# Kernel optimization log

Measured on AMD Instinct MI355X. Metric: run time of the kernel, lower is better.

Reference implementation:

```python
import jax, jax.numpy as jnp
import numpy as np

UNITS = 512
MEM = 16384
IN_DIM = 512
BATCH = 64
USAGE_DECAY = 0.95


def _hard_sigmoid(x):
    # keras hard_sigmoid: clip(0.2*x + 0.5, 0, 1)
    return jnp.clip(0.2 * x + 0.5, 0.0, 1.0)


def _l2norm(x, axis):
    # K.l2_normalize with eps guard
    return x * jax.lax.rsqrt(jnp.maximum(jnp.sum(x * x, axis=axis, keepdims=True), 1e-12))


def setup_inputs() -> dict:
    key = jax.random.key(0)
    ks = jax.random.split(key, 10)
    bias = jnp.concatenate([
        jnp.zeros((UNITS,), jnp.float32),
        jnp.ones((UNITS,), jnp.float32),   # unit_forget_bias
        jnp.zeros((2 * UNITS,), jnp.float32),
    ])
    return {
        "inputs": jax.random.normal(ks[0], (BATCH, IN_DIM), jnp.float32),
        "h_tm1": jax.random.normal(ks[1], (BATCH, UNITS), jnp.float32) * 0.1,
        "c_tm1": jax.random.normal(ks[2], (BATCH, UNITS), jnp.float32) * 0.1,
        "r_tm1": jax.random.normal(ks[3], (BATCH, UNITS), jnp.float32) * 0.1,
        "m_tm1": jax.random.normal(ks[4], (MEM, UNITS), jnp.float32),
        "c_wu_tm1": jax.random.uniform(ks[5], (MEM, BATCH), jnp.float32),
        "c_wlu_tm1": jax.random.uniform(ks[6], (MEM, BATCH), jnp.float32),
        "c_wr_tm1": jax.random.uniform(ks[7], (MEM, BATCH), jnp.float32),
        "kernel": jax.random.normal(ks[8], (IN_DIM, 4 * UNITS), jnp.float32) * 0.02,
        "recurrent_kernel": jax.random.normal(ks[9], (UNITS, 5 * UNITS), jnp.float32) * 0.02,
        "bias": bias,
        "write_gate": jnp.zeros((1,), jnp.float32),
    }


def reference(inputs, h_tm1, c_tm1, r_tm1, m_tm1, c_wu_tm1, c_wlu_tm1, c_wr_tm1,
              kernel, recurrent_kernel, bias, write_gate):
    u = UNITS
    # --- LSTM gates (no dropout / inference path) ---
    x = inputs @ kernel + bias                         # (B, 4U)
    x_i, x_f, x_c, x_o = jnp.split(x, 4, axis=-1)
    hk = h_tm1 @ recurrent_kernel[:, :4 * u]           # (B, 4U)
    h_i, h_f, h_c, h_o = jnp.split(hk, 4, axis=-1)
    r_i = r_tm1 @ recurrent_kernel[:, 4 * u:]          # read vector feeds input gate
    i_g = _hard_sigmoid(x_i + h_i + r_i)
    f_g = _hard_sigmoid(x_f + h_f)
    c = f_g * c_tm1 + i_g * jnp.tanh(x_c + h_c)
    o_g = _hard_sigmoid(x_o + h_o)
    h = o_g * jnp.tanh(c)                              # (B, U)

    # --- external memory addressing ---
    key_list = h.T                                     # (U, B)
    wg = jax.nn.sigmoid(write_gate)                    # (1,)
    # faithful to source: additive c_wlu_tm1 term (no multiply)
    c_ww = wg * c_wr_tm1 + (1.0 - wg) + c_wlu_tm1      # (M, B)
    n_key = _l2norm(key_list, 0)                       # (U, B)
    n_mem = _l2norm(m_tm1, 1)                          # (M, U)
    cos = n_mem @ n_key                                # (M, B)
    # faithful: K.softmax default axis=-1 => softmax over batch axis
    c_wr = jax.nn.softmax(cos, axis=-1)                # (M, B)
    read = (m_tm1.T @ c_wr).T                          # (B, U)
    c_wu = USAGE_DECAY * c_wu_tm1 + c_wr + c_ww        # (M, B)

    # least-used slot per batch column (top_k with k=M, take last => min)
    nth_smallest = jnp.min(c_wu, axis=0)               # (B,)
    nth_smallest_i = jnp.argmin(c_wu, axis=0)          # (B,)
    c_wlu = (c_wu <= nth_smallest[None, :]).astype(jnp.float32)  # (M, B)

    # zero the least-used rows, then write keys weighted by c_ww
    keep = jnp.prod(1.0 - jax.nn.one_hot(nth_smallest_i, MEM, dtype=jnp.float32), axis=0)  # (M,)
    m = m_tm1 * keep[:, None] + c_ww @ h               # (M, U)

    return h, c, read, m, c_wu, c_wlu, c_wr
```

## Files before the change

kernel.cpp:

```cpp
#include <hip/hip_runtime.h>
#include <math.h>

#define OUT_H    0
#define OUT_C    32768
#define OUT_READ 65536
#define OUT_M    98304
#define OUT_CWU  8486912
#define OUT_CWLU 9535488
#define OUT_CWR  10584064

#define WS_NKF   0
#define WS_HBF   16384
#define WS_PMIN  32768
#define WS_PIDX  49152
#define WS_MINF  65536
#define WS_IDXF  65600
#define WS_CWWF  65664
#define WS_CWRF  589952
#define WS_RPART 1114240

typedef short bf16x8 __attribute__((ext_vector_type(8)));
typedef float f32x4  __attribute__((ext_vector_type(4)));

__device__ __forceinline__ float hsig(float x) {
    return fminf(fmaxf(0.2f * x + 0.5f, 0.f), 1.f);
}
__device__ __forceinline__ unsigned short f2bf(float x) {
    unsigned u = __float_as_uint(x);
    return (unsigned short)((u + 0x7fffu + ((u >> 16) & 1u)) >> 16);
}

__global__ __launch_bounds__(256) void k_preact(
    const float* __restrict__ inputs, const float* __restrict__ h_tm1,
    const float* __restrict__ r_tm1, const float* __restrict__ wk,
    const float* __restrict__ rk, float* __restrict__ pre)
{
    __shared__ alignas(16) unsigned short Afr[8192];
    __shared__ alignas(16) unsigned short Bfr[8192];
    const int cb = blockIdx.x % 72, kh = blockIdx.x / 72;
    const int vcol0 = cb * 64;
    const float* A; const float* W; int wstride, wcol0;
    if (vcol0 < 2048)      { A = inputs; W = wk; wstride = 2048; wcol0 = vcol0; }
    else if (vcol0 < 4096) { A = h_tm1;  W = rk; wstride = 2560; wcol0 = vcol0 - 2048; }
    else                   { A = r_tm1;  W = rk; wstride = 2560; wcol0 = 2048 + (vcol0 - 4096); }
    const int tid = threadIdx.x;
    const int w = tid >> 6, lane = tid & 63;
    const int lhi = lane >> 4, llo = lane & 15;

    {
        const int koct = tid & 15;
        const int s = koct >> 2;
        #pragma unroll
        for (int i = 0; i < 4; ++i) {
            int row = i * 16 + (tid >> 4);
            const float* src = &A[row * 512 + kh * 128 + koct * 8];
            float4 x0 = *(const float4*)src;
            float4 x1 = *(const float4*)&src[4];
            int ln = (row & 15) + 16 * (koct & 3);
            int rt = row >> 4;
            union { unsigned short hx[8]; uint4 v; } pk;
            pk.hx[0] = f2bf(x0.x); pk.hx[1] = f2bf(x0.y);
            pk.hx[2] = f2bf(x0.z); pk.hx[3] = f2bf(x0.w);
            pk.hx[4] = f2bf(x1.x); pk.hx[5] = f2bf(x1.y);
            pk.hx[6] = f2bf(x1.z); pk.hx[7] = f2bf(x1.w);
            *(uint4*)&Afr[((s * 4 + rt) * 64 + ln) << 3] = pk.v;
        }
    }
    #pragma unroll
    for (int q = 0; q < 8; ++q) {
        int idx = q * 256 + tid;
        int krow = idx >> 4;
        int c4 = (idx & 15) * 4;
        float4 wv = *(const float4*)&W[(size_t)(kh * 128 + krow) * wstride + wcol0 + c4];
        int s = krow >> 5, lh = (krow & 31) >> 3, e = krow & 7;
        float ws4[4] = { wv.x, wv.y, wv.z, wv.w };
        #pragma unroll
        for (int j = 0; j < 4; ++j) {
            int col = c4 + j;
            int tc = col >> 4;
            int ln = (col & 15) + 16 * lh;
            Bfr[(((s * 4 + tc) * 64 + ln) << 3) + e] = f2bf(ws4[j]);
        }
    }
    __syncthreads();

    f32x4 acc[4] = {};
    #pragma unroll
    for (int s = 0; s < 4; ++s) {
        bf16x8 af = *(const bf16x8*)&Afr[((s * 4 + w) * 64 + lane) << 3];
        #pragma unroll
        for (int tc = 0; tc < 4; ++tc) {
            bf16x8 bf = *(const bf16x8*)&Bfr[((s * 4 + tc) * 64 + lane) << 3];
            acc[tc] = __builtin_amdgcn_mfma_f32_16x16x32_bf16(af, bf, acc[tc], 0, 0, 0);
        }
    }

    float* dst = pre + (size_t)kh * 294912;
    #pragma unroll
    for (int tc = 0; tc < 4; ++tc) {
        #pragma unroll
        for (int reg = 0; reg < 4; ++reg) {
            int row = w * 16 + lhi * 4 + reg;
            dst[row * 4608 + vcol0 + tc * 16 + llo] = acc[tc][reg];
        }
    }
}

__global__ __launch_bounds__(256) void k_gates(
    const float* __restrict__ pre, const float* __restrict__ bias,
    const float* __restrict__ c_tm1, float* __restrict__ out,
    unsigned short* __restrict__ nkf, unsigned short* __restrict__ hbf)
{
    int b = blockIdx.x, t = threadIdx.x;
    const float* p0 = pre + b * 4608;
    const float* p1 = pre + 294912 + b * 4608;
    const float* p2 = pre + 2 * 294912 + b * 4608;
    const float* p3 = pre + 3 * 294912 + b * 4608;
    float hh[2], cc[2];
    #pragma unroll
    for (int q = 0; q < 2; ++q) {
        int u = t + q * 256;
        #define S4(o) (p0[o] + p1[o] + p2[o] + p3[o])
        float xi = S4(u)        + bias[u];
        float xf = S4(512 + u)  + bias[512 + u];
        float xc = S4(1024 + u) + bias[1024 + u];
        float xo = S4(1536 + u) + bias[1536 + u];
        float hi = S4(2048 + u);
        float hf = S4(2560 + u);
        float hc = S4(3072 + u);
        float ho = S4(3584 + u);
        float ri = S4(4096 + u);
        #undef S4
        float ig = hsig(xi + hi + ri);
        float fg = hsig(xf + hf);
        cc[q] = fg * c_tm1[b * 512 + u] + ig * tanhf(xc + hc);
        float og = hsig(xo + ho);
        hh[q] = og * tanhf(cc[q]);
        out[OUT_H + b * 512 + u] = hh[q];
        out[OUT_C + b * 512 + u] = cc[q];
    }
    float ss = hh[0] * hh[0] + hh[1] * hh[1];
    __shared__ float red[4];
    for (int m = 1; m < 64; m <<= 1) ss += __shfl_xor(ss, m);
    if ((t & 63) == 0) red[t >> 6] = ss;
    __syncthreads();
    float tot = red[0] + red[1] + red[2] + red[3];
    float rn = rsqrtf(fmaxf(tot, 1e-12f));
    #pragma unroll
    for (int q = 0; q < 2; ++q) {
        int u = t + q * 256;
        int s = u >> 5, n = b >> 4;
        int lane = (b & 15) + 16 * ((u & 31) >> 3);
        int e = u & 7;
        nkf[(((s * 4 + n) * 64 + lane) << 3) + e] = f2bf(hh[q] * rn);
        int s2 = b >> 5, N = u >> 4;
        int l2 = (u & 15) + 16 * ((b & 31) >> 3);
        int e2 = b & 7;
        hbf[(((s2 * 32 + N) * 64 + l2) << 3) + e2] = f2bf(hh[q]);
    }
}

__global__ __launch_bounds__(256) void k_cos(
    const float* __restrict__ m_tm1, const unsigned short* __restrict__ nkf,
    const float* __restrict__ cwr_tm1, const float* __restrict__ cwlu_tm1,
    const float* __restrict__ cwu_tm1, const float* __restrict__ wgp,
    float* out, float* __restrict__ pmin, int* __restrict__ pidx,
    unsigned short* __restrict__ cwwf, unsigned short* __restrict__ cwrf)
{
    __shared__ alignas(16) unsigned short Af[2048 * 8];
    __shared__ float rn[64];
    __shared__ float pmv[4][64];
    __shared__ int   pmi[4][64];
    const int row0 = blockIdx.x * 64;
    const int tid = threadIdx.x;
    const int w = tid >> 6, lane = tid & 63;
    f32x4 acc[4] = {};
    float ssp[8] = {};

    for (int half = 0; half < 2; ++half) {
        #pragma unroll 2
        for (int i = 0; i < 8; ++i) {
            int r = i * 8 + (tid >> 5);
            int koct = tid & 31;
            const float* src = &m_tm1[(size_t)(row0 + r) * 512 + half * 256 + koct * 8];
            float4 x0 = *(const float4*)src;
            float4 x1 = *(const float4*)&src[4];
            ssp[i] += x0.x*x0.x + x0.y*x0.y + x0.z*x0.z + x0.w*x0.w
                    + x1.x*x1.x + x1.y*x1.y + x1.z*x1.z + x1.w*x1.w;
            int s_l = koct >> 2, rt = r >> 4;
            int ln = ((r & 15) + ((koct & 3) << 4)) ^ (s_l & 7);
            union { unsigned short hx[8]; uint4 v; } pk;
            pk.hx[0] = f2bf(x0.x); pk.hx[1] = f2bf(x0.y);
            pk.hx[2] = f2bf(x0.z); pk.hx[3] = f2bf(x0.w);
            pk.hx[4] = f2bf(x1.x); pk.hx[5] = f2bf(x1.y);
            pk.hx[6] = f2bf(x1.z); pk.hx[7] = f2bf(x1.w);
            *(uint4*)&Af[((s_l * 4 + rt) * 64 + ln) << 3] = pk.v;
        }
        __syncthreads();
        for (int s_l = 0; s_l < 8; ++s_l) {
            int lnx = lane ^ (s_l & 7);
            bf16x8 af = *(const bf16x8*)&Af[((s_l * 4 + w) * 64 + lnx) << 3];
            int s = half * 8 + s_l;
            #pragma unroll
            for (int n = 0; n < 4; ++n) {
                bf16x8 bf = *(const bf16x8*)&nkf[((s * 4 + n) * 64 + lane) << 3];
                acc[n] = __builtin_amdgcn_mfma_f32_16x16x32_bf16(af, bf, acc[n], 0, 0, 0);
            }
        }
        __syncthreads();
    }
    #pragma unroll
    for (int i = 0; i < 8; ++i) {
        float v = ssp[i];
        v += __shfl_xor(v, 1); v += __shfl_xor(v, 2);
        v += __shfl_xor(v, 4); v += __shfl_xor(v, 8);
        v += __shfl_xor(v, 16);
        if ((tid & 31) == 0) rn[i * 8 + (tid >> 5)] = v;
    }
    __syncthreads();

    const float wg = 1.f / (1.f + expf(-wgp[0]));
    const int lhi = lane >> 4, llo = lane & 15;
    float rsq[4];
    #pragma unroll
    for (int reg = 0; reg < 4; ++reg) {
        int rl = w * 16 + lhi * 4 + reg;
        rsq[reg] = rsqrtf(fmaxf(rn[rl], 1e-12f));
    }
    float bmv[4] = { INFINITY, INFINITY, INFINITY, INFINITY };
    int   bmi[4] = { 0x7fffffff, 0x7fffffff, 0x7fffffff, 0x7fffffff };
    #pragma unroll
    for (int reg = 0; reg < 4; ++reg) {
        int rl = w * 16 + lhi * 4 + reg;
        int r = row0 + rl;
        float c0 = acc[0][reg] * rsq[reg];
        float c1 = acc[1][reg] * rsq[reg];
        float c2 = acc[2][reg] * rsq[reg];
        float c3 = acc[3][reg] * rsq[reg];
        float mx = fmaxf(fmaxf(c0, c1), fmaxf(c2, c3));
        mx = fmaxf(mx, __shfl_xor(mx, 1));
        mx = fmaxf(mx, __shfl_xor(mx, 2));
        mx = fmaxf(mx, __shfl_xor(mx, 4));
        mx = fmaxf(mx, __shfl_xor(mx, 8));
        float e0 = expf(c0 - mx), e1 = expf(c1 - mx);
        float e2 = expf(c2 - mx), e3 = expf(c3 - mx);
        float sm = e0 + e1 + e2 + e3;
        sm += __shfl_xor(sm, 1);
        sm += __shfl_xor(sm, 2);
        sm += __shfl_xor(sm, 4);
        sm += __shfl_xor(sm, 8);
        float inv = 1.f / sm;
        float pv[4] = { e0 * inv, e1 * inv, e2 * inv, e3 * inv };
        #pragma unroll
        for (int n = 0; n < 4; ++n) {
            int g = r * 64 + n * 16 + llo;
            float p = pv[n];
            out[OUT_CWR + g] = p;
            float wr = cwr_tm1[g], wl = cwlu_tm1[g], wu = cwu_tm1[g];
            float cww = wg * wr + (1.f - wg) + wl;
            float cwu = 0.95f * wu + p + cww;
            out[OUT_CWU + g] = cwu;
            {
                int rowl16 = lhi * 4 + reg;
                int s2 = n >> 1;
                int l2 = rowl16 + 16 * (((n & 1) << 1) + (llo >> 3));
                Af[(((s2 * 4 + w) * 64 + l2) << 3) + (llo & 7)] = f2bf(cww);
            }
            {
                int sA = rl >> 5;
                int lf = llo + 16 * ((rl & 31) >> 3);
                Af[4096 + (((sA * 4 + n) * 64 + lf) << 3) + (rl & 7)] = f2bf(p);
            }
            if (cwu < bmv[n]) { bmv[n] = cwu; bmi[n] = r; }
        }
    }
    #pragma unroll
    for (int n = 0; n < 4; ++n) {
        #pragma unroll
        for (int mk = 16; mk <= 32; mk <<= 1) {
            float ov = __shfl_xor(bmv[n], mk);
            int   oi = __shfl_xor(bmi[n], mk);
            if (ov < bmv[n] || (ov == bmv[n] && oi < bmi[n])) { bmv[n] = ov; bmi[n] = oi; }
        }
    }
    if (lhi == 0) {
        #pragma unroll
        for (int n = 0; n < 4; ++n) { pmv[w][n * 16 + llo] = bmv[n]; pmi[w][n * 16 + llo] = bmi[n]; }
    }
    __syncthreads();
    {
        uint4* dstW = (uint4*)&cwwf[(size_t)blockIdx.x * 4096];
        uint4* dstR = (uint4*)&cwrf[(size_t)blockIdx.x * 4096];
        const uint4* srcp = (const uint4*)Af;
        dstW[tid]       = srcp[tid];
        dstW[tid + 256] = srcp[tid + 256];
        dstR[tid]       = srcp[512 + tid];
        dstR[tid + 256] = srcp[512 + tid + 256];
    }
    if (tid < 64) {
        float bv = pmv[0][tid]; int bi = pmi[0][tid];
        #pragma unroll
        for (int q = 1; q < 4; ++q) {
            float v = pmv[q][tid]; int i2 = pmi[q][tid];
            if (v < bv || (v == bv && i2 < bi)) { bv = v; bi = i2; }
        }
        pmin[blockIdx.x * 64 + tid] = bv;
        pidx[blockIdx.x * 64 + tid] = bi;
    }
}

__global__ __launch_bounds__(256) void k_read_part(
    const float* __restrict__ m_tm1, const unsigned short* __restrict__ cwrf,
    float* __restrict__ part,
    const float* __restrict__ pmin, const int* __restrict__ pidx,
    float* __restrict__ minf, int* __restrict__ idxf)
{
    __shared__ alignas(16) unsigned short Mf[8192];
    __shared__ float sv[4]; __shared__ int si[4];
    const int bid = blockIdx.x;
    const int tid = threadIdx.x;
    if (bid < 64) {
        int col = bid;
        float bv = pmin[tid * 64 + col];
        int   bi = pidx[tid * 64 + col];
        for (int mk = 1; mk < 64; mk <<= 1) {
            float ov = __shfl_xor(bv, mk);
            int   oi = __shfl_xor(bi, mk);
            if (ov < bv || (ov == bv && oi < bi)) { bv = ov; bi = oi; }
        }
        if ((tid & 63) == 0) { sv[tid >> 6] = bv; si[tid >> 6] = bi; }
        __syncthreads();
        if (tid == 0) {
            #pragma unroll
            for (int q = 1; q < 4; ++q) {
                if (sv[q] < bv || (sv[q] == bv && si[q] < bi)) { bv = sv[q]; bi = si[q]; }
            }
            minf[col] = bv; idxf[col] = bi;
        }
    }
    const int rs = bid >> 3, us = bid & 7;
    const int row0 = rs * 256, u0 = us * 64;
    const int w = tid >> 6, lane = tid & 63;
    f32x4 acc[4] = {};
    for (int ch = 0; ch < 2; ++ch) {
        const int r0 = row0 + ch * 128;
        __syncthreads();
        #pragma unroll
        for (int q = 0; q < 8; ++q) {
            int idx = q * 1024 + tid * 4;
            int rr = idx >> 6, cc = idx & 63;
            float4 mv = *(const float4*)&m_tm1[(size_t)(r0 + rr) * 512 + u0 + cc];
            int s = rr >> 5, e = rr & 7, lo = 16 * ((rr & 31) >> 3);
            float mvs[4] = { mv.x, mv.y, mv.z, mv.w };
            #pragma unroll
            for (int i = 0; i < 4; ++i) {
                int col = cc + i;
                int ln = (col & 15) + lo;
                int t4 = col >> 4;
                Mf[(((s * 4 + t4) * 64 + ln) << 3) + e] = f2bf(mvs[i]);
            }
        }
        __syncthreads();
        const int sgbase = rs * 8 + ch * 4;
        #pragma unroll
        for (int s = 0; s < 4; ++s) {
            bf16x8 bf = *(const bf16x8*)&Mf[((s * 4 + w) * 64 + lane) << 3];
            #pragma unroll
            for (int tb = 0; tb < 4; ++tb) {
                bf16x8 af = *(const bf16x8*)&cwrf[(size_t)((((sgbase + s) * 4 + tb) * 64 + lane)) << 3];
                acc[tb] = __builtin_amdgcn_mfma_f32_16x16x32_bf16(af, bf, acc[tb], 0, 0, 0);
            }
        }
    }
    const int lhi = lane >> 4, llo = lane & 15;
    #pragma unroll
    for (int tb = 0; tb < 4; ++tb) {
        #pragma unroll
        for (int reg = 0; reg < 4; ++reg) {
            int b = tb * 16 + lhi * 4 + reg;
            part[(size_t)rs * 32768 + b * 512 + u0 + w * 16 + llo] = acc[tb][reg];
        }
    }
}

__global__ __launch_bounds__(256) void k_update(
    const float* __restrict__ m_tm1, const unsigned short* __restrict__ cwwf,
    const unsigned short* __restrict__ hbf,
    const float* __restrict__ minf, const int* __restrict__ idxf,
    const float* __restrict__ rpart, float* out)
{
    __shared__ float keepf[64];
    __shared__ float minS[64];
    __shared__ int   idxS[64];
    const int rb = blockIdx.x >> 2, us = blockIdx.x & 3;
    const int row0 = rb * 64, u0 = us * 128;
    const int tid = threadIdx.x;
    const int w = tid >> 6, lane = tid & 63;
    const int lhi = lane >> 4, llo = lane & 15;
    if (tid < 64) { idxS[tid] = idxf[tid]; minS[tid] = minf[tid]; }
    __syncthreads();
    if (tid < 64) {
        int gr = row0 + tid;
        float f = 1.f;
        #pragma unroll
        for (int b = 0; b < 64; ++b) if (idxS[b] == gr) f = 0.f;
        keepf[tid] = f;
    }
    __syncthreads();
    if (us == 0) {
        #pragma unroll
        for (int q = 0; q < 4; ++q) {
            int idx = q * 1024 + tid * 4;
            int r = idx >> 6, b = idx & 63;
            int g = (row0 + r) * 64 + b;
            float4 cu = *(const float4*)&out[OUT_CWU + g];
            float4 res;
            res.x = (cu.x <= minS[b + 0]) ? 1.f : 0.f;
            res.y = (cu.y <= minS[b + 1]) ? 1.f : 0.f;
            res.z = (cu.z <= minS[b + 2]) ? 1.f : 0.f;
            res.w = (cu.w <= minS[b + 3]) ? 1.f : 0.f;
            *(float4*)&out[OUT_CWLU + g] = res;
        }
    } else if (us == 1) {
        if (tid < 128) {
            int gid = rb * 128 + tid;
            float s = 0.f;
            #pragma unroll 8
            for (int rs = 0; rs < 64; ++rs) s += rpart[(size_t)rs * 32768 + gid];
            out[OUT_READ + gid] = s;
        }
    }
    f32x4 acc[8];
    #pragma unroll
    for (int nt = 0; nt < 8; ++nt) {
        #pragma unroll
        for (int reg = 0; reg < 4; ++reg) {
            int rowl = w * 16 + lhi * 4 + reg;
            acc[nt][reg] = m_tm1[(size_t)(row0 + rowl) * 512 + u0 + nt * 16 + llo]
                         * keepf[rowl];
        }
    }
    #pragma unroll
    for (int s = 0; s < 2; ++s) {
        bf16x8 af = *(const bf16x8*)&cwwf[(size_t)rb * 4096 + (((s * 4 + w) * 64 + lane) << 3)];
        #pragma unroll
        for (int nt = 0; nt < 8; ++nt) {
            int N = (u0 >> 4) + nt;
            bf16x8 bf = *(const bf16x8*)&hbf[((s * 32 + N) * 64 + lane) << 3];
            acc[nt] = __builtin_amdgcn_mfma_f32_16x16x32_bf16(af, bf, acc[nt], 0, 0, 0);
        }
    }
    #pragma unroll
    for (int nt = 0; nt < 8; ++nt) {
        #pragma unroll
        for (int reg = 0; reg < 4; ++reg) {
            int rowl = w * 16 + lhi * 4 + reg;
            out[OUT_M + (size_t)(row0 + rowl) * 512 + u0 + nt * 16 + llo] = acc[nt][reg];
        }
    }
}

extern "C" void kernel_launch(void* const* d_in, const int* in_sizes, int n_in,
                              void* d_out, int out_size, void* d_ws, size_t ws_size,
                              hipStream_t stream)
{
    const float* inputs    = (const float*)d_in[0];
    const float* h_tm1     = (const float*)d_in[1];
    const float* c_tm1     = (const float*)d_in[2];
    const float* r_tm1     = (const float*)d_in[3];
    const float* m_tm1     = (const float*)d_in[4];
    const float* c_wu_tm1  = (const float*)d_in[5];
    const float* c_wlu_tm1 = (const float*)d_in[6];
    const float* c_wr_tm1  = (const float*)d_in[7];
    const float* wk        = (const float*)d_in[8];
    const float* rk        = (const float*)d_in[9];
    const float* bias      = (const float*)d_in[10];
    const float* wgate     = (const float*)d_in[11];
    float* out = (float*)d_out;
    float* ws  = (float*)d_ws;
    float* pre = out + OUT_M;
    unsigned short* nkf  = (unsigned short*)(ws + WS_NKF);
    unsigned short* hbf  = (unsigned short*)(ws + WS_HBF);
    unsigned short* cwwf = (unsigned short*)(ws + WS_CWWF);
    unsigned short* cwrf = (unsigned short*)(ws + WS_CWRF);
    float* rpart = ws + WS_RPART;

    k_preact<<<288, 256, 0, stream>>>(inputs, h_tm1, r_tm1, wk, rk, pre);
    k_gates<<<64, 256, 0, stream>>>(pre, bias, c_tm1, out, nkf, hbf);
    k_cos<<<256, 256, 0, stream>>>(m_tm1, nkf, c_wr_tm1, c_wlu_tm1,
                                   c_wu_tm1, wgate, out, ws + WS_PMIN,
                                   (int*)(ws + WS_PIDX), cwwf, cwrf);
    k_read_part<<<512, 256, 0, stream>>>(m_tm1, cwrf, rpart,
                                         ws + WS_PMIN, (const int*)(ws + WS_PIDX),
                                         ws + WS_MINF, (int*)(ws + WS_IDXF));
    k_update<<<1024, 256, 0, stream>>>(m_tm1, cwwf, hbf,
                                       ws + WS_MINF, (const int*)(ws + WS_IDXF),
                                       rpart, out);
}
```

Baseline: 62.38 us.

## Split k_cos K-reduction across 8 waves with single-pass staging

k_cos now runs 512 threads per block. It loads the whole 64x512 memory tile into LDS in one pass instead of two halves, and splits the MFMA K loop between two wave groups whose partial accumulators are summed through shared memory. The goal is more memory-level parallelism and shorter per-wave MFMA chains, which should help hide the global load latency for m_tm1. In exchange it uses roughly twice the LDS (about 80KB per block), which may lower occupancy. It also adds a reduction barrier and leaves half the waves idle during the softmax epilogue.

```diff
diff --git a/kernel.cpp b/kernel.cpp
--- a/kernel.cpp
+++ b/kernel.cpp
@@ -160,14 +160,15 @@
     }
 }
 
-__global__ __launch_bounds__(256) void k_cos(
+__global__ __launch_bounds__(512) void k_cos(
     const float* __restrict__ m_tm1, const unsigned short* __restrict__ nkf,
     const float* __restrict__ cwr_tm1, const float* __restrict__ cwlu_tm1,
     const float* __restrict__ cwu_tm1, const float* __restrict__ wgp,
     float* out, float* __restrict__ pmin, int* __restrict__ pidx,
     unsigned short* __restrict__ cwwf, unsigned short* __restrict__ cwrf)
 {
-    __shared__ alignas(16) unsigned short Af[2048 * 8];
+    __shared__ alignas(16) unsigned short Af[4096 * 8];
+    __shared__ alignas(16) float redacc[4][4][64][4];
     __shared__ float rn[64];
     __shared__ float pmv[4][64];
     __shared__ int   pmi[4][64];
@@ -177,125 +178,138 @@
     f32x4 acc[4] = {};
     float ssp[8] = {};
 
-    for (int half = 0; half < 2; ++half) {
-        #pragma unroll 2
-        for (int i = 0; i < 8; ++i) {
-            int r = i * 8 + (tid >> 5);
-            int koct = tid & 31;
-            const float* src = &m_tm1[(size_t)(row0 + r) * 512 + half * 256 + koct * 8];
-            float4 x0 = *(const float4*)src;
-            float4 x1 = *(const float4*)&src[4];
-            ssp[i] += x0.x*x0.x + x0.y*x0.y + x0.z*x0.z + x0.w*x0.w
-                    + x1.x*x1.x + x1.y*x1.y + x1.z*x1.z + x1.w*x1.w;
-            int s_l = koct >> 2, rt = r >> 4;
-            int ln = ((r & 15) + ((koct & 3) << 4)) ^ (s_l & 7);
-            union { unsigned short hx[8]; uint4 v; } pk;
-            pk.hx[0] = f2bf(x0.x); pk.hx[1] = f2bf(x0.y);
-            pk.hx[2] = f2bf(x0.z); pk.hx[3] = f2bf(x0.w);
-            pk.hx[4] = f2bf(x1.x); pk.hx[5] = f2bf(x1.y);
-            pk.hx[6] = f2bf(x1.z); pk.hx[7] = f2bf(x1.w);
-            *(uint4*)&Af[((s_l * 4 + rt) * 64 + ln) << 3] = pk.v;
-        }
-        __syncthreads();
+    #pragma unroll
+    for (int i = 0; i < 8; ++i) {
+        int r = i * 8 + w;
+        int koct = lane;
+        const float* src = &m_tm1[(size_t)(row0 + r) * 512 + koct * 8];
+        float4 x0 = *(const float4*)src;
+        float4 x1 = *(const float4*)&src[4];
+        ssp[i] += x0.x*x0.x + x0.y*x0.y + x0.z*x0.z + x0.w*x0.w
+                + x1.x*x1.x + x1.y*x1.y + x1.z*x1.z + x1.w*x1.w;
+        int s_l = koct >> 2, rt = r >> 4;
+        int ln = ((r & 15) + ((koct & 3) << 4)) ^ (s_l & 7);
+        union { unsigned short hx[8]; uint4 v; } pk;
+        pk.hx[0] = f2bf(x0.x); pk.hx[1] = f2bf(x0.y);
+        pk.hx[2] = f2bf(x0.z); pk.hx[3] = f2bf(x0.w);
+        pk.hx[4] = f2bf(x1.x); pk.hx[5] = f2bf(x1.y);
+        pk.hx[6] = f2bf(x1.z); pk.hx[7] = f2bf(x1.w);
+        *(uint4*)&Af[((s_l * 4 + rt) * 64 + ln) << 3] = pk.v;
+    }
+    #pragma unroll
+    for (int i = 0; i < 8; ++i) {
+        float v = ssp[i];
+        v += __shfl_xor(v, 1); v += __shfl_xor(v, 2);
+        v += __shfl_xor(v, 4); v += __shfl_xor(v, 8);
+        v += __shfl_xor(v, 16); v += __shfl_xor(v, 32);
+        if (lane == 0) rn[i * 8 + w] = v;
+    }
+    __syncthreads();
+
+    {
+        const int wt = w & 3, kh2 = w >> 2;
         for (int s_l = 0; s_l < 8; ++s_l) {
-            int lnx = lane ^ (s_l & 7);
-            bf16x8 af = *(const bf16x8*)&Af[((s_l * 4 + w) * 64 + lnx) << 3];
-            int s = half * 8 + s_l;
+            int s = kh2 * 8 + s_l;
+            int lnx = lane ^ (s & 7);
+            bf16x8 af = *(const bf16x8*)&Af[((s * 4 + wt) * 64 + lnx) << 3];
             #pragma unroll
             for (int n = 0; n < 4; ++n) {
                 bf16x8 bf = *(const bf16x8*)&nkf[((s * 4 + n) * 64 + lane) << 3];
                 acc[n] = __builtin_amdgcn_mfma_f32_16x16x32_bf16(af, bf, acc[n], 0, 0, 0);
             }
         }
-        __syncthreads();
-    }
-    #pragma unroll
-    for (int i = 0; i < 8; ++i) {
-        float v = ssp[i];
-        v += __shfl_xor(v, 1); v += __shfl_xor(v, 2);
-        v += __shfl_xor(v, 4); v += __shfl_xor(v, 8);
-        v += __shfl_xor(v, 16);
-        if ((tid & 31) == 0) rn[i * 8 + (tid >> 5)] = v;
-    }
-    __syncthreads();
+    }
+    if (w >= 4) {
+        #pragma unroll
+        for (int n = 0; n < 4; ++n)
+            *(f32x4*)&redacc[w - 4][n][lane][0] = acc[n];
+    }
+    __syncthreads();
+    if (w < 4) {
+        #pragma unroll
+        for (int n = 0; n < 4; ++n) {
+            f32x4 o = *(const f32x4*)&redacc[w][n][lane][0];
+            acc[n][0] += o[0]; acc[n][1] += o[1]; acc[n][2] += o[2]; acc[n][3] += o[3];
+        }
+    }
 
     const float wg = 1.f / (1.f + expf(-wgp[0]));
     const int lhi = lane >> 4, llo = lane & 15;
-    float rsq[4];
-    #pragma unroll
-    for (int reg = 0; reg < 4; ++reg) {
-        int rl = w * 16 + lhi * 4 + reg;
-        rsq[reg] = rsqrtf(fmaxf(rn[rl], 1e-12f));
-    }
-    float bmv[4] = { INFINITY, INFINITY, INFINITY, INFINITY };
-    int   bmi[4] = { 0x7fffffff, 0x7fffffff, 0x7fffffff, 0x7fffffff };
-    #pragma unroll
-    for (int reg = 0; reg < 4; ++reg) {
-        int rl = w * 16 + lhi * 4 + reg;
-        int r = row0 + rl;
-        float c0 = acc[0][reg] * rsq[reg];
-        float c1 = acc[1][reg] * rsq[reg];
-        float c2 = acc[2][reg] * rsq[reg];
-        float c3 = acc[3][reg] * rsq[reg];
-        float mx = fmaxf(fmaxf(c0, c1), fmaxf(c2, c3));
-        mx = fmaxf(mx, __shfl_xor(mx, 1));
-        mx = fmaxf(mx, __shfl_xor(mx, 2));
-        mx = fmaxf(mx, __shfl_xor(mx, 4));
-        mx = fmaxf(mx, __shfl_xor(mx, 8));
-        float e0 = expf(c0 - mx), e1 = expf(c1 - mx);
-        float e2 = expf(c2 - mx), e3 = expf(c3 - mx);
-        float sm = e0 + e1 + e2 + e3;
-        sm += __shfl_xor(sm, 1);
-        sm += __shfl_xor(sm, 2);
-        sm += __shfl_xor(sm, 4);
-        sm += __shfl_xor(sm, 8);
-        float inv = 1.f / sm;
-        float pv[4] = { e0 * inv, e1 * inv, e2 * inv, e3 * inv };
+    if (w < 4) {
+        float rsq[4];
+        #pragma unroll
+        for (int reg = 0; reg < 4; ++reg) {
+            int rl = w * 16 + lhi * 4 + reg;
+            rsq[reg] = rsqrtf(fmaxf(rn[rl], 1e-12f));
+        }
+        float bmv[4] = { INFINITY, INFINITY, INFINITY, INFINITY };
+        int   bmi[4] = { 0x7fffffff, 0x7fffffff, 0x7fffffff, 0x7fffffff };
+        #pragma unroll
+        for (int reg = 0; reg < 4; ++reg) {
+            int rl = w * 16 + lhi * 4 + reg;
+            int r = row0 + rl;
+            float c0 = acc[0][reg] * rsq[reg];
+            float c1 = acc[1][reg] * rsq[reg];
+            float c2 = acc[2][reg] * rsq[reg];
+            float c3 = acc[3][reg] * rsq[reg];
+            float mx = fmaxf(fmaxf(c0, c1), fmaxf(c2, c3));
+            mx = fmaxf(mx, __shfl_xor(mx, 1));
+            mx = fmaxf(mx, __shfl_xor(mx, 2));
+            mx = fmaxf(mx, __shfl_xor(mx, 4));
+            mx = fmaxf(mx, __shfl_xor(mx, 8));
+            float e0 = expf(c0 - mx), e1 = expf(c1 - mx);
+            float e2 = expf(c2 - mx), e3 = expf(c3 - mx);
+            float sm = e0 + e1 + e2 + e3;
+            sm += __shfl_xor(sm, 1);
+            sm += __shfl_xor(sm, 2);
+            sm += __shfl_xor(sm, 4);
+            sm += __shfl_xor(sm, 8);
+            float inv = 1.f / sm;
+            float pv[4] = { e0 * inv, e1 * inv, e2 * inv, e3 * inv };
+            #pragma unroll
+            for (int n = 0; n < 4; ++n) {
+                int g = r * 64 + n * 16 + llo;
+                float p = pv[n];
+                out[OUT_CWR + g] = p;
+                float wr = cwr_tm1[g], wl = cwlu_tm1[g], wu = cwu_tm1[g];
+                float cww = wg * wr + (1.f - wg) + wl;
+                float cwu = 0.95f * wu + p + cww;
+                out[OUT_CWU + g] = cwu;
+                {
+                    int rowl16 = lhi * 4 + reg;
+                    int s2 = n >> 1;
+                    int l2 = rowl16 + 16 * (((n & 1) << 1) + (llo >> 3));
+                    Af[(((s2 * 4 + w) * 64 + l2) << 3) + (llo & 7)] = f2bf(cww);
+                }
+                {
+                    int sA = rl >> 5;
+                    int lf = llo + 16 * ((rl & 31) >> 3);
+                    Af[4096 + (((sA * 4 + n) * 64 + lf) << 3) + (rl & 7)] = f2bf(p);
+                }
+                if (cwu < bmv[n]) { bmv[n] = cwu; bmi[n] = r; }
+            }
+        }
         #pragma unroll
         for (int n = 0; n < 4; ++n) {
-            int g = r * 64 + n * 16 + llo;
-            float p = pv[n];
-            out[OUT_CWR + g] = p;
-            float wr = cwr_tm1[g], wl = cwlu_tm1[g], wu = cwu_tm1[g];
-            float cww = wg * wr + (1.f - wg) + wl;
-            float cwu = 0.95f * wu + p + cww;
-            out[OUT_CWU + g] = cwu;
-            {
-                int rowl16 = lhi * 4 + reg;
-                int s2 = n >> 1;
-                int l2 = rowl16 + 16 * (((n & 1) << 1) + (llo >> 3));
-                Af[(((s2 * 4 + w) * 64 + l2) << 3) + (llo & 7)] = f2bf(cww);
+            #pragma unroll
+            for (int mk = 16; mk <= 32; mk <<= 1) {
+                float ov = __shfl_xor(bmv[n], mk);
+                int   oi = __shfl_xor(bmi[n], mk);
+                if (ov < bmv[n] || (ov == bmv[n] && oi < bmi[n])) { bmv[n] = ov; bmi[n] = oi; }
             }
-            {
-                int sA = rl >> 5;
-                int lf = llo + 16 * ((rl & 31) >> 3);
-                Af[4096 + (((sA * 4 + n) * 64 + lf) << 3) + (rl & 7)] = f2bf(p);
-            }
-            if (cwu < bmv[n]) { bmv[n] = cwu; bmi[n] = r; }
-        }
-    }
-    #pragma unroll
-    for (int n = 0; n < 4; ++n) {
-        #pragma unroll
-        for (int mk = 16; mk <= 32; mk <<= 1) {
-            float ov = __shfl_xor(bmv[n], mk);
-            int   oi = __shfl_xor(bmi[n], mk);
-            if (ov < bmv[n] || (ov == bmv[n] && oi < bmi[n])) { bmv[n] = ov; bmi[n] = oi; }
-        }
-    }
-    if (lhi == 0) {
-        #pragma unroll
-        for (int n = 0; n < 4; ++n) { pmv[w][n * 16 + llo] = bmv[n]; pmi[w][n * 16 + llo] = bmi[n]; }
+        }
+        if (lhi == 0) {
+            #pragma unroll
+            for (int n = 0; n < 4; ++n) { pmv[w][n * 16 + llo] = bmv[n]; pmi[w][n * 16 + llo] = bmi[n]; }
+        }
     }
     __syncthreads();
     {
         uint4* dstW = (uint4*)&cwwf[(size_t)blockIdx.x * 4096];
         uint4* dstR = (uint4*)&cwrf[(size_t)blockIdx.x * 4096];
         const uint4* srcp = (const uint4*)Af;
-        dstW[tid]       = srcp[tid];
-        dstW[tid + 256] = srcp[tid + 256];
-        dstR[tid]       = srcp[512 + tid];
-        dstR[tid + 256] = srcp[512 + tid + 256];
+        dstW[tid] = srcp[tid];
+        dstR[tid] = srcp[512 + tid];
     }
     if (tid < 64) {
         float bv = pmv[0][tid]; int bi = pmi[0][tid];
@@ -487,7 +501,7 @@
 
     k_preact<<<288, 256, 0, stream>>>(inputs, h_tm1, r_tm1, wk, rk, pre);
     k_gates<<<64, 256, 0, stream>>>(pre, bias, c_tm1, out, nkf, hbf);
-    k_cos<<<256, 256, 0, stream>>>(m_tm1, nkf, c_wr_tm1, c_wlu_tm1,
+    k_cos<<<256, 512, 0, stream>>>(m_tm1, nkf, c_wr_tm1, c_wlu_tm1,
                                    c_wu_tm1, wgate, out, ws + WS_PMIN,
                                    (int*)(ws + WS_PIDX), cwwf, cwrf);
     k_read_part<<<512, 256, 0, stream>>>(m_tm1, cwrf, rpart,
```

Result: faster. 59.48 us (median of 2 runs) (-4.7%).
